# Optimization experiments

Hardware: AMD Instinct MI355X
Metric: run time of the kernel (lower is better)

The kernel has to match this reference:

```python
import jax, jax.numpy as jnp
import numpy as np

B, H, S, D = 4, 16, 4096, 64

def _phi(x):
    # feature map for linear attention: elu(x) + 1 (positive features)
    return jax.nn.elu(x) + 1.0

def setup_inputs() -> dict:
    key = jax.random.key(0)
    kq, kk, kv = jax.random.split(key, 3)
    return {
        "query": jax.random.normal(kq, (B, H, S, D), dtype=jnp.float32),
        "key": jax.random.normal(kk, (B, H, S, D), dtype=jnp.float32),
        "value": jax.random.normal(kv, (B, H, S, D), dtype=jnp.float32),
        "attention_mask": jnp.ones((B, S), dtype=jnp.float32),
    }

def reference(query, key, value, attention_mask):
    head_dim = query.shape[-1]
    scale = 1.0 / jnp.sqrt(jnp.sqrt(jnp.float32(head_dim)))
    q = query * scale
    k = key * scale
    phi_q = _phi(q)
    phi_k = _phi(k)
    m = attention_mask[:, None, :, None]  # [B,1,S,1]
    phi_q = phi_q * m
    phi_k = phi_k * m
    # kv_term: [B,H,D,Dv]
    kv_term = jnp.einsum("bhsd,bhse->bhde", phi_k, value)
    out = jnp.einsum("bhsd,bhde->bhse", phi_q, kv_term)
    # normalizer: phi_q @ sum_s phi_k -> [B,H,S,1]
    k_one = jnp.sum(phi_k, axis=-2)  # [B,H,D]
    normalizer = jnp.einsum("bhsd,bhd->bhs", phi_q, k_one)[..., None]
    return out / (normalizer + 1e-8)
```

## Files before the change

### kernel.cpp

```cpp
#include <hip/hip_runtime.h>

#define BDIM 4
#define HDIM 16
#define SDIM 4096
#define DDIM 64
#define NBH (BDIM * HDIM)

#define BH_STRIDE (DDIM * DDIM + DDIM)
#define CHUNK_FLOATS (NBH * BH_STRIDE)

#define P1_STRIDE 66
#define P1_WSZ (2 * 16 * P1_STRIDE)

__device__ __forceinline__ float phi_f(float x) {
    return x > 0.0f ? x + 1.0f : __expf(x);
}

template<bool ATOMIC>
__global__ __launch_bounds__(128) void la_phase1(
    const float* __restrict__ K, const float* __restrict__ V,
    const float* __restrict__ mask, float* __restrict__ outp, int chunk_rows)
{
    __shared__ float smem[2 * P1_WSZ + 64];

    const int bh = blockIdx.y;
    const int b  = bh / HDIM;
    const int t  = threadIdx.x;
    const int w  = t >> 6;
    const int l  = t & 63;

    float* kTw = smem + w * P1_WSZ;
    float* vTw = kTw + 16 * P1_STRIDE;
    float* k1w = smem + 2 * P1_WSZ;

    const int lr = l & 15;
    const int cg = (l >> 4) << 2;
    const int d0 = (l >> 3) << 3;
    const int e0 = (l & 7) << 3;

    const int rows_per_wave = chunk_rows >> 1;
    const int s_wave = blockIdx.x * chunk_rows + w * rows_per_wave;
    const int ntiles = rows_per_wave >> 4;

    const float* Kb = K + (size_t)bh * SDIM * DDIM;
    const float* Vb = V + (size_t)bh * SDIM * DDIM;
    const float* mb = mask + (size_t)b * SDIM;

    const float scale = 0.35355339059327373f;

    float acc[8][8] = {};
    float k1p[4][4] = {};

    float4 kf[4], vf[4];
    float m;
    {
        const int sr = s_wave + lr;
        #pragma unroll
        for (int j = 0; j < 4; ++j) {
            kf[j] = *(const float4*)(Kb + (size_t)sr * DDIM + cg + 16 * j);
            vf[j] = *(const float4*)(Vb + (size_t)sr * DDIM + cg + 16 * j);
        }
        m = mb[sr];
    }

    for (int tt = 0; tt < ntiles; ++tt) {
        float p[4][4];
        #pragma unroll
        for (int j = 0; j < 4; ++j) {
            p[j][0] = phi_f(kf[j].x * scale) * m;
            p[j][1] = phi_f(kf[j].y * scale) * m;
            p[j][2] = phi_f(kf[j].z * scale) * m;
            p[j][3] = phi_f(kf[j].w * scale) * m;
            k1p[j][0] += p[j][0]; k1p[j][1] += p[j][1];
            k1p[j][2] += p[j][2]; k1p[j][3] += p[j][3];
        }
        {
            float* kw = kTw + lr * P1_STRIDE;
            float* vw = vTw + lr * P1_STRIDE;
            #pragma unroll
            for (int j = 0; j < 4; ++j) {
                const int c = cg + 16 * j;
                *(float2*)(kw + c)     = make_float2(p[j][0], p[j][1]);
                *(float2*)(kw + c + 2) = make_float2(p[j][2], p[j][3]);
                *(float2*)(vw + c)     = make_float2(vf[j].x, vf[j].y);
                *(float2*)(vw + c + 2) = make_float2(vf[j].z, vf[j].w);
            }
        }
        if (tt + 1 < ntiles) {
            const int sr = s_wave + ((tt + 1) << 4) + lr;
            #pragma unroll
            for (int j = 0; j < 4; ++j) {
                kf[j] = *(const float4*)(Kb + (size_t)sr * DDIM + cg + 16 * j);
                vf[j] = *(const float4*)(Vb + (size_t)sr * DDIM + cg + 16 * j);
            }
            m = mb[sr];
        }
        #pragma unroll
        for (int ss = 0; ss < 16; ++ss) {
            float a[8], v[8];
            const float* kr = kTw + ss * P1_STRIDE + d0;
            const float* vr = vTw + ss * P1_STRIDE + e0;
            *(float2*)&a[0] = *(const float2*)(kr);
            *(float2*)&a[2] = *(const float2*)(kr + 2);
            *(float2*)&a[4] = *(const float2*)(kr + 4);
            *(float2*)&a[6] = *(const float2*)(kr + 6);
            *(float2*)&v[0] = *(const float2*)(vr);
            *(float2*)&v[2] = *(const float2*)(vr + 2);
            *(float2*)&v[4] = *(const float2*)(vr + 4);
            *(float2*)&v[6] = *(const float2*)(vr + 6);
            #pragma unroll
            for (int i = 0; i < 8; ++i)
                #pragma unroll
                for (int j = 0; j < 8; ++j)
                    acc[i][j] += a[i] * v[j];
        }
    }

    #pragma unroll
    for (int j = 0; j < 4; ++j)
        #pragma unroll
        for (int jj = 0; jj < 4; ++jj)
            kTw[lr * P1_STRIDE + cg + 16 * j + jj] = k1p[j][jj];
    float k1s = 0.f;
    #pragma unroll
    for (int r = 0; r < 16; ++r) k1s += kTw[r * P1_STRIDE + l];

    __syncthreads();
    float4* flat = (float4*)smem;
    if (w == 1) {
        #pragma unroll
        for (int i = 0; i < 16; ++i) {
            const int r = i >> 1, h = (i & 1) << 2;
            flat[i * 64 + l] = make_float4(acc[r][h], acc[r][h + 1], acc[r][h + 2], acc[r][h + 3]);
        }
        k1w[l] = k1s;
    }
    __syncthreads();
    if (w == 0) {
        float* base = ATOMIC ? (outp + (size_t)bh * BH_STRIDE)
                             : (outp + ((size_t)blockIdx.x * NBH + bh) * BH_STRIDE);
        #pragma unroll
        for (int i = 0; i < 16; ++i) {
            const int r = i >> 1, h = (i & 1) << 2;
            float4 o = flat[i * 64 + l];
            o.x += acc[r][h]; o.y += acc[r][h + 1]; o.z += acc[r][h + 2]; o.w += acc[r][h + 3];
            if (ATOMIC) {
                float* p = base + (d0 + r) * DDIM + e0 + h;
                atomicAdd(p + 0, o.x); atomicAdd(p + 1, o.y);
                atomicAdd(p + 2, o.z); atomicAdd(p + 3, o.w);
            } else {
                *(float4*)(base + (d0 + r) * DDIM + e0 + h) = o;
            }
        }
        const float k1tot = k1s + k1w[l];
        if (ATOMIC) atomicAdd(&base[DDIM * DDIM + l], k1tot);
        else        base[DDIM * DDIM + l] = k1tot;
    }
}

__global__ __launch_bounds__(256) void la_reduce(
    const float* __restrict__ part, float* __restrict__ fin, int nc)
{
    const int g = blockIdx.x * 256 + threadIdx.x;
    const float4* p4 = (const float4*)part;
    float4 s = p4[g];
    for (int c = 1; c < nc; ++c) {
        const float4 v = p4[(size_t)c * (CHUNK_FLOATS / 4) + g];
        s.x += v.x; s.y += v.y; s.z += v.z; s.w += v.w;
    }
    ((float4*)fin)[g] = s;
}

__global__ __launch_bounds__(128) void la_phase2(
    const float* __restrict__ Q, const float* __restrict__ mask,
    const float* __restrict__ fin_all, float* __restrict__ out)
{
    __shared__ float kvL[DDIM * DDIM];
    __shared__ float pqT[DDIM * 132];
    __shared__ float koL[DDIM];

    const int bh = blockIdx.y;
    const int b  = bh / HDIM;
    const int t  = threadIdx.x;
    const int s_base = blockIdx.x * 128;

    const float scale = 0.35355339059327373f;
    const float* fin = fin_all + (size_t)bh * BH_STRIDE;

    {
        const float4* src = (const float4*)fin;
        float4* dst = (float4*)kvL;
        #pragma unroll
        for (int i = 0; i < 8; ++i) dst[t + 128 * i] = src[t + 128 * i];
        if (t < DDIM) koL[t] = fin[DDIM * DDIM + t];
    }
    {
        const float* Qb = Q + (size_t)bh * SDIM * DDIM;
        const float* mb = mask + (size_t)b * SDIM;
        #pragma unroll
        for (int j = 0; j < 16; ++j) {
            const int row = (t & 15) + ((j & 7) << 4);
            const int c4  = ((t >> 4) << 2) + ((j >> 3) << 5);
            const float4 qf = *(const float4*)(Qb + (size_t)(s_base + row) * DDIM + c4);
            const float mm = mb[s_base + row];
            pqT[(c4 + 0) * 132 + row] = phi_f(qf.x * scale) * mm;
            pqT[(c4 + 1) * 132 + row] = phi_f(qf.y * scale) * mm;
            pqT[(c4 + 2) * 132 + row] = phi_f(qf.z * scale) * mm;
            pqT[(c4 + 3) * 132 + row] = phi_f(qf.w * scale) * mm;
        }
    }
    __syncthreads();

    const int r0 = (t >> 3) << 3;
    const int e0 = (t & 7) << 3;
    float acc[8][8] = {};
    float nrm[8] = {};

    #pragma unroll 4
    for (int d = 0; d < DDIM; ++d) {
        float a[8], bb[8];
        *(float4*)&a[0]  = *(const float4*)(pqT + d * 132 + r0);
        *(float4*)&a[4]  = *(const float4*)(pqT + d * 132 + r0 + 4);
        *(float4*)&bb[0] = *(const float4*)(kvL + d * DDIM + e0);
        *(float4*)&bb[4] = *(const float4*)(kvL + d * DDIM + e0 + 4);
        const float ko = koL[d];
        #pragma unroll
        for (int i = 0; i < 8; ++i) {
            nrm[i] += a[i] * ko;
            #pragma unroll
            for (int j = 0; j < 8; ++j) acc[i][j] += a[i] * bb[j];
        }
    }

    float* ob = out + ((size_t)bh * SDIM + s_base) * DDIM;
    #pragma unroll
    for (int i = 0; i < 8; ++i) {
        const float inv = 1.0f / (nrm[i] + 1e-8f);
        *(float4*)(ob + (size_t)(r0 + i) * DDIM + e0) =
            make_float4(acc[i][0] * inv, acc[i][1] * inv, acc[i][2] * inv, acc[i][3] * inv);
        *(float4*)(ob + (size_t)(r0 + i) * DDIM + e0 + 4) =
            make_float4(acc[i][4] * inv, acc[i][5] * inv, acc[i][6] * inv, acc[i][7] * inv);
    }
}

extern "C" void kernel_launch(void* const* d_in, const int* in_sizes, int n_in,
                              void* d_out, int out_size, void* d_ws, size_t ws_size,
                              hipStream_t stream) {
    const float* Q = (const float*)d_in[0];
    const float* K = (const float*)d_in[1];
    const float* V = (const float*)d_in[2];
    const float* M = (const float*)d_in[3];
    float* out = (float*)d_out;

    const size_t chunk_bytes = (size_t)CHUNK_FLOATS * sizeof(float);

    int nc = 0;
    if      (ws_size >= 33 * chunk_bytes) nc = 32;
    else if (ws_size >= 17 * chunk_bytes) nc = 16;

    if (nc > 0) {
        float* part = (float*)d_ws;
        float* fin  = part + (size_t)nc * CHUNK_FLOATS;
        la_phase1<false><<<dim3(nc, NBH), dim3(128), 0, stream>>>(K, V, M, part, SDIM / nc);
        la_reduce<<<dim3(CHUNK_FLOATS / 4 / 256), dim3(256), 0, stream>>>(part, fin, nc);
        la_phase2<<<dim3(SDIM / 128, NBH), dim3(128), 0, stream>>>(Q, M, fin, out);
    } else {
        float* fin = (float*)d_ws;
        hipMemsetAsync(d_ws, 0, chunk_bytes, stream);
        la_phase1<true><<<dim3(16, NBH), dim3(128), 0, stream>>>(K, V, M, fin, SDIM / 16);
        la_phase2<<<dim3(SDIM / 128, NBH), dim3(128), 0, stream>>>(Q, M, fin, out);
    }
}
```

Baseline: 266.3 us.

## Drop LDS staging in both phases; read K/V/Q fragments directly into registers

Phase 1 no longer stages phi(K) and V tiles through LDS. Each lane loads its own 8-wide K and V slices per row straight from global memory, with a one-row register prefetch, and accumulates the outer product and the k-sum in registers. Phase 2 drops the transposed phi(Q) LDS tile and moves to 256 threads, each computing 4 rows by 8 columns and streaming Q in 4-column chunks from global memory. This removes LDS traffic and barriers, but it relies on redundant global loads (each K/V/Q element is read by 8 lanes) being served by the cache, and on poorly coalesced per-lane access patterns.

```diff
diff --git a/kernel.cpp b/kernel.cpp
--- a/kernel.cpp
+++ b/kernel.cpp
@@ -9,152 +9,111 @@
 #define BH_STRIDE (DDIM * DDIM + DDIM)
 #define CHUNK_FLOATS (NBH * BH_STRIDE)
 
-#define P1_STRIDE 66
-#define P1_WSZ (2 * 16 * P1_STRIDE)
-
 __device__ __forceinline__ float phi_f(float x) {
     return x > 0.0f ? x + 1.0f : __expf(x);
 }
 
 template<bool ATOMIC>
-__global__ __launch_bounds__(128) void la_phase1(
+__global__ __launch_bounds__(128, 3) void la_phase1(
     const float* __restrict__ K, const float* __restrict__ V,
     const float* __restrict__ mask, float* __restrict__ outp, int chunk_rows)
 {
-    __shared__ float smem[2 * P1_WSZ + 64];
+    __shared__ float comb[DDIM * DDIM];
+    __shared__ float combk1[DDIM];
 
     const int bh = blockIdx.y;
     const int b  = bh / HDIM;
     const int t  = threadIdx.x;
     const int w  = t >> 6;
     const int l  = t & 63;
-
-    float* kTw = smem + w * P1_WSZ;
-    float* vTw = kTw + 16 * P1_STRIDE;
-    float* k1w = smem + 2 * P1_WSZ;
-
-    const int lr = l & 15;
-    const int cg = (l >> 4) << 2;
     const int d0 = (l >> 3) << 3;
     const int e0 = (l & 7) << 3;
 
-    const int rows_per_wave = chunk_rows >> 1;
-    const int s_wave = blockIdx.x * chunk_rows + w * rows_per_wave;
-    const int ntiles = rows_per_wave >> 4;
+    const int rpw = chunk_rows >> 1;
+    const int s0  = blockIdx.x * chunk_rows + w * rpw;
 
     const float* Kb = K + (size_t)bh * SDIM * DDIM;
     const float* Vb = V + (size_t)bh * SDIM * DDIM;
     const float* mb = mask + (size_t)b * SDIM;
-
     const float scale = 0.35355339059327373f;
 
     float acc[8][8] = {};
-    float k1p[4][4] = {};
-
-    float4 kf[4], vf[4];
-    float m;
-    {
-        const int sr = s_wave + lr;
-        #pragma unroll
-        for (int j = 0; j < 4; ++j) {
-            kf[j] = *(const float4*)(Kb + (size_t)sr * DDIM + cg + 16 * j);
-            vf[j] = *(const float4*)(Vb + (size_t)sr * DDIM + cg + 16 * j);
-        }
-        m = mb[sr];
-    }
-
-    for (int tt = 0; tt < ntiles; ++tt) {
-        float p[4][4];
-        #pragma unroll
-        for (int j = 0; j < 4; ++j) {
-            p[j][0] = phi_f(kf[j].x * scale) * m;
-            p[j][1] = phi_f(kf[j].y * scale) * m;
-            p[j][2] = phi_f(kf[j].z * scale) * m;
-            p[j][3] = phi_f(kf[j].w * scale) * m;
-            k1p[j][0] += p[j][0]; k1p[j][1] += p[j][1];
-            k1p[j][2] += p[j][2]; k1p[j][3] += p[j][3];
-        }
-        {
-            float* kw = kTw + lr * P1_STRIDE;
-            float* vw = vTw + lr * P1_STRIDE;
-            #pragma unroll
-            for (int j = 0; j < 4; ++j) {
-                const int c = cg + 16 * j;
-                *(float2*)(kw + c)     = make_float2(p[j][0], p[j][1]);
-                *(float2*)(kw + c + 2) = make_float2(p[j][2], p[j][3]);
-                *(float2*)(vw + c)     = make_float2(vf[j].x, vf[j].y);
-                *(float2*)(vw + c + 2) = make_float2(vf[j].z, vf[j].w);
-            }
-        }
-        if (tt + 1 < ntiles) {
-            const int sr = s_wave + ((tt + 1) << 4) + lr;
-            #pragma unroll
-            for (int j = 0; j < 4; ++j) {
-                kf[j] = *(const float4*)(Kb + (size_t)sr * DDIM + cg + 16 * j);
-                vf[j] = *(const float4*)(Vb + (size_t)sr * DDIM + cg + 16 * j);
-            }
-            m = mb[sr];
-        }
-        #pragma unroll
-        for (int ss = 0; ss < 16; ++ss) {
-            float a[8], v[8];
-            const float* kr = kTw + ss * P1_STRIDE + d0;
-            const float* vr = vTw + ss * P1_STRIDE + e0;
-            *(float2*)&a[0] = *(const float2*)(kr);
-            *(float2*)&a[2] = *(const float2*)(kr + 2);
-            *(float2*)&a[4] = *(const float2*)(kr + 4);
-            *(float2*)&a[6] = *(const float2*)(kr + 6);
-            *(float2*)&v[0] = *(const float2*)(vr);
-            *(float2*)&v[2] = *(const float2*)(vr + 2);
-            *(float2*)&v[4] = *(const float2*)(vr + 4);
-            *(float2*)&v[6] = *(const float2*)(vr + 6);
-            #pragma unroll
-            for (int i = 0; i < 8; ++i)
-                #pragma unroll
-                for (int j = 0; j < 8; ++j)
-                    acc[i][j] += a[i] * v[j];
-        }
-    }
-
-    #pragma unroll
-    for (int j = 0; j < 4; ++j)
-        #pragma unroll
-        for (int jj = 0; jj < 4; ++jj)
-            kTw[lr * P1_STRIDE + cg + 16 * j + jj] = k1p[j][jj];
-    float k1s = 0.f;
-    #pragma unroll
-    for (int r = 0; r < 16; ++r) k1s += kTw[r * P1_STRIDE + l];
+    float k1[8] = {};
+
+    float4 ka0 = *(const float4*)(Kb + (size_t)s0 * DDIM + d0);
+    float4 ka1 = *(const float4*)(Kb + (size_t)s0 * DDIM + d0 + 4);
+    float4 va0 = *(const float4*)(Vb + (size_t)s0 * DDIM + e0);
+    float4 va1 = *(const float4*)(Vb + (size_t)s0 * DDIM + e0 + 4);
+    float  mc  = mb[s0];
+
+    #pragma unroll 2
+    for (int i = 0; i < rpw; ++i) {
+        const int sn = s0 + ((i + 1 < rpw) ? (i + 1) : i);
+        const float4 kb0 = *(const float4*)(Kb + (size_t)sn * DDIM + d0);
+        const float4 kb1 = *(const float4*)(Kb + (size_t)sn * DDIM + d0 + 4);
+        const float4 vb0 = *(const float4*)(Vb + (size_t)sn * DDIM + e0);
+        const float4 vb1 = *(const float4*)(Vb + (size_t)sn * DDIM + e0 + 4);
+        const float  mn  = mb[sn];
+
+        float a[8], v[8];
+        a[0] = phi_f(ka0.x * scale) * mc;  a[1] = phi_f(ka0.y * scale) * mc;
+        a[2] = phi_f(ka0.z * scale) * mc;  a[3] = phi_f(ka0.w * scale) * mc;
+        a[4] = phi_f(ka1.x * scale) * mc;  a[5] = phi_f(ka1.y * scale) * mc;
+        a[6] = phi_f(ka1.z * scale) * mc;  a[7] = phi_f(ka1.w * scale) * mc;
+        v[0] = va0.x; v[1] = va0.y; v[2] = va0.z; v[3] = va0.w;
+        v[4] = va1.x; v[5] = va1.y; v[6] = va1.z; v[7] = va1.w;
+
+        #pragma unroll
+        for (int x = 0; x < 8; ++x) k1[x] += a[x];
+
+        #pragma unroll
+        for (int x = 0; x < 8; ++x)
+            #pragma unroll
+            for (int y = 0; y < 8; ++y)
+                acc[x][y] += a[x] * v[y];
+
+        ka0 = kb0; ka1 = kb1; va0 = vb0; va1 = vb1; mc = mn;
+    }
 
     __syncthreads();
-    float4* flat = (float4*)smem;
     if (w == 1) {
         #pragma unroll
-        for (int i = 0; i < 16; ++i) {
-            const int r = i >> 1, h = (i & 1) << 2;
-            flat[i * 64 + l] = make_float4(acc[r][h], acc[r][h + 1], acc[r][h + 2], acc[r][h + 3]);
-        }
-        k1w[l] = k1s;
+        for (int i = 0; i < 8; ++i) {
+            *(float4*)&comb[(d0 + i) * DDIM + e0]     = make_float4(acc[i][0], acc[i][1], acc[i][2], acc[i][3]);
+            *(float4*)&comb[(d0 + i) * DDIM + e0 + 4] = make_float4(acc[i][4], acc[i][5], acc[i][6], acc[i][7]);
+        }
+        if (e0 == 0) {
+            #pragma unroll
+            for (int i = 0; i < 8; ++i) combk1[d0 + i] = k1[i];
+        }
     }
     __syncthreads();
     if (w == 0) {
         float* base = ATOMIC ? (outp + (size_t)bh * BH_STRIDE)
                              : (outp + ((size_t)blockIdx.x * NBH + bh) * BH_STRIDE);
         #pragma unroll
-        for (int i = 0; i < 16; ++i) {
-            const int r = i >> 1, h = (i & 1) << 2;
-            float4 o = flat[i * 64 + l];
-            o.x += acc[r][h]; o.y += acc[r][h + 1]; o.z += acc[r][h + 2]; o.w += acc[r][h + 3];
+        for (int i = 0; i < 8; ++i) {
+            float4 o0 = *(const float4*)&comb[(d0 + i) * DDIM + e0];
+            float4 o1 = *(const float4*)&comb[(d0 + i) * DDIM + e0 + 4];
+            o0.x += acc[i][0]; o0.y += acc[i][1]; o0.z += acc[i][2]; o0.w += acc[i][3];
+            o1.x += acc[i][4]; o1.y += acc[i][5]; o1.z += acc[i][6]; o1.w += acc[i][7];
             if (ATOMIC) {
-                float* p = base + (d0 + r) * DDIM + e0 + h;
-                atomicAdd(p + 0, o.x); atomicAdd(p + 1, o.y);
-                atomicAdd(p + 2, o.z); atomicAdd(p + 3, o.w);
+                float* p = base + (d0 + i) * DDIM + e0;
+                atomicAdd(p + 0, o0.x); atomicAdd(p + 1, o0.y); atomicAdd(p + 2, o0.z); atomicAdd(p + 3, o0.w);
+                atomicAdd(p + 4, o1.x); atomicAdd(p + 5, o1.y); atomicAdd(p + 6, o1.z); atomicAdd(p + 7, o1.w);
             } else {
-                *(float4*)(base + (d0 + r) * DDIM + e0 + h) = o;
+                *(float4*)(base + (d0 + i) * DDIM + e0)     = o0;
+                *(float4*)(base + (d0 + i) * DDIM + e0 + 4) = o1;
             }
         }
-        const float k1tot = k1s + k1w[l];
-        if (ATOMIC) atomicAdd(&base[DDIM * DDIM + l], k1tot);
-        else        base[DDIM * DDIM + l] = k1tot;
+        if (e0 == 0) {
+            #pragma unroll
+            for (int i = 0; i < 8; ++i) {
+                const float k1t = k1[i] + combk1[d0 + i];
+                if (ATOMIC) atomicAdd(&base[DDIM * DDIM + d0 + i], k1t);
+                else        base[DDIM * DDIM + d0 + i] = k1t;
+            }
+        }
     }
 }
 
@@ -171,12 +130,11 @@
     ((float4*)fin)[g] = s;
 }
 
-__global__ __launch_bounds__(128) void la_phase2(
+__global__ __launch_bounds__(256, 4) void la_phase2(
     const float* __restrict__ Q, const float* __restrict__ mask,
     const float* __restrict__ fin_all, float* __restrict__ out)
 {
     __shared__ float kvL[DDIM * DDIM];
-    __shared__ float pqT[DDIM * 132];
     __shared__ float koL[DDIM];
 
     const int bh = blockIdx.y;
@@ -191,55 +149,68 @@
         const float4* src = (const float4*)fin;
         float4* dst = (float4*)kvL;
         #pragma unroll
-        for (int i = 0; i < 8; ++i) dst[t + 128 * i] = src[t + 128 * i];
+        for (int i = 0; i < 4; ++i) dst[t + 256 * i] = src[t + 256 * i];
         if (t < DDIM) koL[t] = fin[DDIM * DDIM + t];
     }
-    {
-        const float* Qb = Q + (size_t)bh * SDIM * DDIM;
-        const float* mb = mask + (size_t)b * SDIM;
-        #pragma unroll
-        for (int j = 0; j < 16; ++j) {
-            const int row = (t & 15) + ((j & 7) << 4);
-            const int c4  = ((t >> 4) << 2) + ((j >> 3) << 5);
-            const float4 qf = *(const float4*)(Qb + (size_t)(s_base + row) * DDIM + c4);
-            const float mm = mb[s_base + row];
-            pqT[(c4 + 0) * 132 + row] = phi_f(qf.x * scale) * mm;
-            pqT[(c4 + 1) * 132 + row] = phi_f(qf.y * scale) * mm;
-            pqT[(c4 + 2) * 132 + row] = phi_f(qf.z * scale) * mm;
-            pqT[(c4 + 3) * 132 + row] = phi_f(qf.w * scale) * mm;
-        }
-    }
     __syncthreads();
 
-    const int r0 = (t >> 3) << 3;
     const int e0 = (t & 7) << 3;
-    float acc[8][8] = {};
-    float nrm[8] = {};
-
-    #pragma unroll 4
-    for (int d = 0; d < DDIM; ++d) {
-        float a[8], bb[8];
-        *(float4*)&a[0]  = *(const float4*)(pqT + d * 132 + r0);
-        *(float4*)&a[4]  = *(const float4*)(pqT + d * 132 + r0 + 4);
-        *(float4*)&bb[0] = *(const float4*)(kvL + d * DDIM + e0);
-        *(float4*)&bb[4] = *(const float4*)(kvL + d * DDIM + e0 + 4);
-        const float ko = koL[d];
-        #pragma unroll
-        for (int i = 0; i < 8; ++i) {
-            nrm[i] += a[i] * ko;
-            #pragma unroll
-            for (int j = 0; j < 8; ++j) acc[i][j] += a[i] * bb[j];
-        }
-    }
-
-    float* ob = out + ((size_t)bh * SDIM + s_base) * DDIM;
+    const int r0 = (t >> 3) << 2;
+    const float* Qb = Q + (size_t)bh * SDIM * DDIM;
+    const float* mb = mask + (size_t)b * SDIM;
+    const size_t rowoff = (size_t)(s_base + r0) * DDIM;
+
+    float mrow[4];
     #pragma unroll
-    for (int i = 0; i < 8; ++i) {
-        const float inv = 1.0f / (nrm[i] + 1e-8f);
-        *(float4*)(ob + (size_t)(r0 + i) * DDIM + e0) =
-            make_float4(acc[i][0] * inv, acc[i][1] * inv, acc[i][2] * inv, acc[i][3] * inv);
-        *(float4*)(ob + (size_t)(r0 + i) * DDIM + e0 + 4) =
-            make_float4(acc[i][4] * inv, acc[i][5] * inv, acc[i][6] * inv, acc[i][7] * inv);
+    for (int j = 0; j < 4; ++j) mrow[j] = mb[s_base + r0 + j];
+
+    float acc[4][8] = {};
+    float nrm[4] = {};
+
+    float4 qa[4];
+    #pragma unroll
+    for (int j = 0; j < 4; ++j) qa[j] = *(const float4*)(Qb + rowoff + j * DDIM);
+
+    for (int dc = 0; dc < DDIM; dc += 4) {
+        const int dn = (dc + 4 < DDIM) ? (dc + 4) : dc;
+        float4 qb[4];
+        #pragma unroll
+        for (int j = 0; j < 4; ++j) qb[j] = *(const float4*)(Qb + rowoff + j * DDIM + dn);
+
+        float a[4][4];
+        #pragma unroll
+        for (int j = 0; j < 4; ++j) {
+            a[j][0] = phi_f(qa[j].x * scale) * mrow[j];
+            a[j][1] = phi_f(qa[j].y * scale) * mrow[j];
+            a[j][2] = phi_f(qa[j].z * scale) * mrow[j];
+            a[j][3] = phi_f(qa[j].w * scale) * mrow[j];
+        }
+
+        #pragma unroll
+        for (int dd = 0; dd < 4; ++dd) {
+            const float ko = koL[dc + dd];
+            float bb[8];
+            *(float4*)&bb[0] = *(const float4*)&kvL[(dc + dd) * DDIM + e0];
+            *(float4*)&bb[4] = *(const float4*)&kvL[(dc + dd) * DDIM + e0 + 4];
+            #pragma unroll
+            for (int j = 0; j < 4; ++j) {
+                nrm[j] += a[j][dd] * ko;
+                #pragma unroll
+                for (int x = 0; x < 8; ++x) acc[j][x] += a[j][dd] * bb[x];
+            }
+        }
+        #pragma unroll
+        for (int j = 0; j < 4; ++j) qa[j] = qb[j];
+    }
+
+    float* ob = out + ((size_t)bh * SDIM + s_base + r0) * DDIM;
+    #pragma unroll
+    for (int j = 0; j < 4; ++j) {
+        const float inv = 1.0f / (nrm[j] + 1e-8f);
+        *(float4*)(ob + (size_t)j * DDIM + e0) =
+            make_float4(acc[j][0] * inv, acc[j][1] * inv, acc[j][2] * inv, acc[j][3] * inv);
+        *(float4*)(ob + (size_t)j * DDIM + e0 + 4) =
+            make_float4(acc[j][4] * inv, acc[j][5] * inv, acc[j][6] * inv, acc[j][7] * inv);
     }
 }
 
@@ -263,11 +234,11 @@
         float* fin  = part + (size_t)nc * CHUNK_FLOATS;
         la_phase1<false><<<dim3(nc, NBH), dim3(128), 0, stream>>>(K, V, M, part, SDIM / nc);
         la_reduce<<<dim3(CHUNK_FLOATS / 4 / 256), dim3(256), 0, stream>>>(part, fin, nc);
-        la_phase2<<<dim3(SDIM / 128, NBH), dim3(128), 0, stream>>>(Q, M, fin, out);
+        la_phase2<<<dim3(SDIM / 128, NBH), dim3(256), 0, stream>>>(Q, M, fin, out);
     } else {
         float* fin = (float*)d_ws;
         hipMemsetAsync(d_ws, 0, chunk_bytes, stream);
         la_phase1<true><<<dim3(16, NBH), dim3(128), 0, stream>>>(K, V, M, fin, SDIM / 16);
-        la_phase2<<<dim3(SDIM / 128, NBH), dim3(128), 0, stream>>>(Q, M, fin, out);
-    }
-}
+        la_phase2<<<dim3(SDIM / 128, NBH), dim3(256), 0, stream>>>(Q, M, fin, out);
+    }
+}
```

Measured after the change: 295.7 us. 11.1% more time.
